# Kernel optimization log

Hardware: AMD Instinct MI355X
Metric: run time of the kernel (lower is better)

The kernel has to match this reference:

```python
import jax, jax.numpy as jnp
import numpy as np

N, E = 50000, 600000
IN_DIM, HID, OUT = 512, 256, 64
NEG_SLOPE = 0.2  # pyg GATConv default negative_slope


def setup_inputs() -> dict:
    key = jax.random.key(0)
    ks = jax.random.split(key, 6)
    features = jax.random.normal(ks[0], (N, IN_DIM), jnp.float32)
    edge_index = jax.random.randint(ks[1], (2, E), 0, N)
    W1 = jax.random.normal(ks[2], (IN_DIM, HID), jnp.float32) * (1.0 / np.sqrt(IN_DIM))
    W2 = jax.random.normal(ks[3], (HID, OUT), jnp.float32) * (1.0 / np.sqrt(HID))
    att_src = jax.random.normal(ks[4], (HID,), jnp.float32) * 0.1
    att_dst = jax.random.normal(ks[5], (HID,), jnp.float32) * 0.1
    return {"features": features, "W1": W1, "W2": W2,
            "att_src": att_src, "att_dst": att_dst, "edge_index": edge_index}


def _gat_propagate(h_pre, a_src, a_dst, src, dst, n):
    """STAGATE GATConv message passing (heads=1, concat=False, no self loops).

    Per-edge logit = leaky_relu(alpha_src[src] + alpha_dst[dst]),
    softmax over edges sharing the same dst, scatter-add of weighted src feats.
    """
    logits = jax.nn.leaky_relu(a_src[src] + a_dst[dst], NEG_SLOPE)        # [E]
    m = jax.ops.segment_max(logits, dst, num_segments=n)                   # [N]
    ex = jnp.exp(logits - m[dst])                                          # [E]
    denom = jax.ops.segment_sum(ex, dst, num_segments=n)                   # [N]
    w = ex / (denom[dst] + 1e-16)                                          # [E], pyg softmax eps
    return jax.ops.segment_sum(h_pre[src] * w[:, None], dst, num_segments=n)  # [N, C]


def reference(features, W1, W2, att_src, att_dst, edge_index):
    src, dst = edge_index[0], edge_index[1]
    n = features.shape[0]
    # conv1: attention computed and cached (self.attentions)
    hp1 = features @ W1                      # [N, HID]
    a_s = hp1 @ att_src                      # [N] per-node src attention score
    a_d = hp1 @ att_dst                      # [N] per-node dst attention score
    h1 = jax.nn.elu(_gat_propagate(hp1, a_s, a_d, src, dst, n))
    # conv2: attention=False -> plain linear
    h2 = h1 @ W2                             # [N, OUT]
    # conv3: weights = conv2.lin_src.T, tied_attention = conv1.attentions
    hp3 = h2 @ W2.T                          # [N, HID]
    h3 = jax.nn.elu(_gat_propagate(hp3, a_s, a_d, src, dst, n))
    # conv4: weights = conv1.lin_src.T, attention=False
    h4 = h3 @ W1.T                           # [N, IN_DIM]
    return (h2, h4)
```

## Files before the change

### kernel.cpp

```cpp
#include <hip/hip_runtime.h>
#include <hip/hip_bf16.h>
#include <cstdint>
#include <cstddef>

#define IN_DIM 512
#define HID 256
#define OUTD 64
#define NEG_SLOPE 0.2f

typedef __attribute__((ext_vector_type(8))) __bf16 bfrag_t;
typedef __attribute__((ext_vector_type(4))) float facc_t;
typedef __attribute__((ext_vector_type(4))) unsigned int u32x4;

__device__ __forceinline__ float bf2f(unsigned short u) {
  return __uint_as_float(((unsigned int)u) << 16);
}
__device__ __forceinline__ unsigned short f2bf(float f) {
  unsigned int x = __float_as_uint(f);
  x = (x + 0x7FFFu + ((x >> 16) & 1u)) >> 16;
  return (unsigned short)x;
}

#define GLOAD_LDS16(g, l)                                              \
  __builtin_amdgcn_global_load_lds(                                    \
      (const __attribute__((address_space(1))) void*)(g),              \
      (__attribute__((address_space(3))) void*)(l), 16, 0, 0)

template <int BM, int BN>
__global__ __launch_bounds__(256) void gemm_bt(const unsigned short* __restrict__ A,
                                               const unsigned short* __restrict__ B,
                                               void* __restrict__ Craw,
                                               unsigned short* __restrict__ Cb,
                                               int M, int N, int K, int c32, int act) {
  constexpr int FM = BM / 32, FN = BN / 32;
  constexpr int RT = BM + BN;
  __shared__ __align__(16) unsigned short lds[RT * 32];

  const int bm0 = blockIdx.x * BM;
  const int bn0 = blockIdx.y * BN;
  const int tid = threadIdx.x;
  const int lane = tid & 63;
  const int wave = tid >> 6;
  const int wrow = (wave >> 1) * (BM / 2);
  const int wcol = (wave & 1) * (BN / 2);
  const int lr = lane & 15;
  const int quad = lane >> 4;
  const int swz = (quad ^ (lr & 3)) << 3;

  facc_t acc[FM][FN];
#pragma unroll
  for (int i = 0; i < FM; ++i)
#pragma unroll
    for (int j = 0; j < FN; ++j) acc[i][j] = (facc_t){0.f, 0.f, 0.f, 0.f};

  for (int k0 = 0; k0 < K; k0 += 32) {
    __syncthreads();
#pragma unroll
    for (int t = wave; t < RT / 16; t += 4) {
      const int r0 = t * 16;
      const int row = r0 + (lane >> 2);
      const int seg = (lane & 3) ^ (row & 3);
      const unsigned short* g;
      if (r0 < BM) {
        int gm = bm0 + row;
        if (gm >= M) gm = M - 1;
        g = A + (size_t)gm * K + k0 + seg * 8;
      } else {
        g = B + (size_t)(bn0 + row - BM) * K + k0 + seg * 8;
      }
      GLOAD_LDS16(g, lds + t * 512);
    }
    __syncthreads();

    bfrag_t a[FM], b[FN];
#pragma unroll
    for (int i = 0; i < FM; ++i)
      a[i] = *(const bfrag_t*)&lds[(wrow + i * 16 + lr) * 32 + swz];
#pragma unroll
    for (int j = 0; j < FN; ++j)
      b[j] = *(const bfrag_t*)&lds[(BM + wcol + j * 16 + lr) * 32 + swz];
#pragma unroll
    for (int i = 0; i < FM; ++i)
#pragma unroll
      for (int j = 0; j < FN; ++j)
        acc[i][j] = __builtin_amdgcn_mfma_f32_16x16x32_bf16(a[i], b[j], acc[i][j], 0, 0, 0);
  }

#pragma unroll
  for (int i = 0; i < FM; ++i)
#pragma unroll
    for (int r = 0; r < 4; ++r) {
      const int grow = bm0 + wrow + i * 16 + quad * 4 + r;
      if (grow < M) {
#pragma unroll
        for (int j = 0; j < FN; ++j) {
          const int gcol = bn0 + wcol + j * 16 + lr;
          float v = acc[i][j][r];
          if (act) v = v > 0.f ? v : (expf(v) - 1.f);
          if (c32) ((float*)Craw)[(size_t)grow * N + gcol] = v;
          else ((unsigned short*)Craw)[(size_t)grow * N + gcol] = f2bf(v);
          if (Cb) Cb[(size_t)grow * N + gcol] = f2bf(v);
        }
      }
    }
}

template <int BM, int BN>
__global__ __launch_bounds__(256) void gemm_a32_bt_att(const float* __restrict__ A,
                                                       const unsigned short* __restrict__ B,
                                                       unsigned short* __restrict__ C,
                                                       const float* __restrict__ att_s,
                                                       const float* __restrict__ att_d,
                                                       float* __restrict__ as_,
                                                       float* __restrict__ ad_,
                                                       int M, int N, int K) {
  constexpr int FM = BM / 32, FN = BN / 32;
  constexpr int RT = BM + BN;
  __shared__ __align__(16) unsigned short lds[RT * 32];

  const int bm0 = blockIdx.x * BM;
  const int tid = threadIdx.x;
  const int lane = tid & 63;
  const int wave = tid >> 6;
  const int wrow = (wave >> 1) * (BM / 2);
  const int wcol = (wave & 1) * (BN / 2);
  const int lr = lane & 15;
  const int quad = lane >> 4;
  const int swz = (quad ^ (lr & 3)) << 3;

  const int arow0 = tid >> 2;
  const int aseg = tid & 3;

  facc_t acc[FM][FN];
#pragma unroll
  for (int i = 0; i < FM; ++i)
#pragma unroll
    for (int j = 0; j < FN; ++j) acc[i][j] = (facc_t){0.f, 0.f, 0.f, 0.f};

  for (int k0 = 0; k0 < K; k0 += 32) {
    __syncthreads();
#pragma unroll
    for (int t = wave; t < BN / 16; t += 4) {
      const int lr0 = BM + t * 16;
      const int row = lr0 + (lane >> 2);
      const int seg = (lane & 3) ^ (row & 3);
      const unsigned short* g = B + (size_t)(t * 16 + (lane >> 2)) * K + k0 + seg * 8;
      GLOAD_LDS16(g, lds + lr0 * 32);
    }
#pragma unroll
    for (int h = 0; h < 2; ++h) {
      const int row = arow0 + h * (BM / 2);
      int gm = bm0 + row;
      if (gm >= M) gm = M - 1;
      const float* g = A + (size_t)gm * K + k0 + aseg * 8;
      const float4 fa = ((const float4*)g)[0];
      const float4 fb = ((const float4*)g)[1];
      u32x4 pk;
      pk.x = (unsigned int)f2bf(fa.x) | ((unsigned int)f2bf(fa.y) << 16);
      pk.y = (unsigned int)f2bf(fa.z) | ((unsigned int)f2bf(fa.w) << 16);
      pk.z = (unsigned int)f2bf(fb.x) | ((unsigned int)f2bf(fb.y) << 16);
      pk.w = (unsigned int)f2bf(fb.z) | ((unsigned int)f2bf(fb.w) << 16);
      *(u32x4*)&lds[row * 32 + ((aseg ^ (row & 3)) << 3)] = pk;
    }
    __syncthreads();

    bfrag_t a[FM], b[FN];
#pragma unroll
    for (int i = 0; i < FM; ++i)
      a[i] = *(const bfrag_t*)&lds[(wrow + i * 16 + lr) * 32 + swz];
#pragma unroll
    for (int j = 0; j < FN; ++j)
      b[j] = *(const bfrag_t*)&lds[(BM + wcol + j * 16 + lr) * 32 + swz];
#pragma unroll
    for (int i = 0; i < FM; ++i)
#pragma unroll
      for (int j = 0; j < FN; ++j)
        acc[i][j] = __builtin_amdgcn_mfma_f32_16x16x32_bf16(a[i], b[j], acc[i][j], 0, 0, 0);
  }

  float av_s[FN], av_d[FN];
#pragma unroll
  for (int j = 0; j < FN; ++j) {
    av_s[j] = att_s[wcol + j * 16 + lr];
    av_d[j] = att_d[wcol + j * 16 + lr];
  }
  float* redS = (float*)lds;
  float* redD = (float*)lds + 2 * BM;
  __syncthreads();

#pragma unroll
  for (int i = 0; i < FM; ++i)
#pragma unroll
    for (int r = 0; r < 4; ++r) {
      const int grow = bm0 + wrow + i * 16 + quad * 4 + r;
      float ps = 0.f, pd = 0.f;
#pragma unroll
      for (int j = 0; j < FN; ++j) {
        const float v = acc[i][j][r];
        ps += v * av_s[j];
        pd += v * av_d[j];
        if (grow < M) C[(size_t)grow * N + (wcol + j * 16 + lr)] = f2bf(v);
      }
      ps += __shfl_xor(ps, 1); ps += __shfl_xor(ps, 2);
      ps += __shfl_xor(ps, 4); ps += __shfl_xor(ps, 8);
      pd += __shfl_xor(pd, 1); pd += __shfl_xor(pd, 2);
      pd += __shfl_xor(pd, 4); pd += __shfl_xor(pd, 8);
      if (lr == 0) {
        const int rloc = wrow + i * 16 + quad * 4 + r;
        redS[(wave & 1) * BM + rloc] = ps;
        redD[(wave & 1) * BM + rloc] = pd;
      }
    }
  __syncthreads();
  if (tid < BM) {
    const int grow = bm0 + tid;
    if (grow < M) {
      as_[grow] = redS[tid] + redS[BM + tid];
      ad_[grow] = redD[tid] + redD[BM + tid];
    }
  }
}

__global__ void cvt_weights(const float* __restrict__ W1, const float* __restrict__ W2,
                            unsigned short* __restrict__ W1T, unsigned short* __restrict__ W1b,
                            unsigned short* __restrict__ W2T, unsigned short* __restrict__ W2b) {
  const int idx = blockIdx.x * 256 + threadIdx.x;
  if (idx < IN_DIM * HID) {
    const unsigned short b = f2bf(W1[idx]);
    W1b[idx] = b;
    const int r = idx >> 8, c = idx & 255;
    W1T[(size_t)c * IN_DIM + r] = b;
  }
  if (idx < HID * OUTD) {
    const unsigned short b = f2bf(W2[idx]);
    W2b[idx] = b;
    const int r = idx >> 6, c = idx & 63;
    W2T[(size_t)c * HID + r] = b;
  }
}

__global__ void init_deg(int* __restrict__ deg, int n) {
  const int i = blockIdx.x * 256 + threadIdx.x;
  if (i < n) deg[i] = 0;
}

__global__ void edge_pass1(const int* __restrict__ src, const int* __restrict__ dst,
                           const float* __restrict__ as_, const float* __restrict__ ad_,
                           float* __restrict__ eexp, int* __restrict__ deg, int E, int n) {
  const int e = blockIdx.x * 256 + threadIdx.x;
  if (e >= E) return;
  const int s = src[e], d = dst[e];
  if ((unsigned)s >= (unsigned)n || (unsigned)d >= (unsigned)n) return;
  float l = as_[s] + ad_[d];
  l = l > 0.f ? l : NEG_SLOPE * l;
  eexp[e] = expf(fminf(l, 60.f));
  atomicAdd(&deg[d], 1);
}

__global__ __launch_bounds__(256) void scan_reduce(const int* __restrict__ deg,
                                                   int* __restrict__ bsum, int n) {
  __shared__ int ws4[4];
  const int tid = threadIdx.x, lane = tid & 63, wid = tid >> 6;
  const int base = blockIdx.x * 2048 + tid * 8;
  int s = 0;
#pragma unroll
  for (int j = 0; j < 8; ++j) {
    const int i = base + j;
    if (i < n) s += deg[i];
  }
  for (int off = 32; off > 0; off >>= 1) s += __shfl_down(s, off);
  if (lane == 0) ws4[wid] = s;
  __syncthreads();
  if (tid == 0) bsum[blockIdx.x] = ws4[0] + ws4[1] + ws4[2] + ws4[3];
}

__global__ __launch_bounds__(256) void scan_final(const int* __restrict__ deg,
                                                  const int* __restrict__ bsum,
                                                  int* __restrict__ row_ptr,
                                                  int* __restrict__ cursor, int n) {
  __shared__ int wsum[4];
  __shared__ int blockoff;
  const int tid = threadIdx.x, lane = tid & 63, wid = tid >> 6;
  if (wid == 0) {
    int v = (lane < blockIdx.x) ? bsum[lane] : 0;
    for (int off = 32; off > 0; off >>= 1) v += __shfl_down(v, off);
    if (lane == 0) blockoff = v;
  }
  const int base = blockIdx.x * 2048 + tid * 8;
  int v[8], s = 0;
#pragma unroll
  for (int j = 0; j < 8; ++j) {
    const int i = base + j;
    v[j] = (i < n) ? deg[i] : 0;
    s += v[j];
  }
  int ws = s;
  for (int off = 1; off < 64; off <<= 1) {
    const int t = __shfl_up(ws, off);
    if (lane >= off) ws += t;
  }
  if (lane == 63) wsum[wid] = ws;
  __syncthreads();
  int woff = 0;
  for (int w_ = 0; w_ < wid; ++w_) woff += wsum[w_];
  int run = blockoff + woff + (ws - s);
#pragma unroll
  for (int j = 0; j < 8; ++j) {
    const int i = base + j;
    if (i < n) {
      cursor[i] = run;
      row_ptr[i + 1] = run + v[j];
    }
    run += v[j];
  }
  if (blockIdx.x == 0 && tid == 0) row_ptr[0] = 0;
}

__global__ void edge_scatter(const int* __restrict__ src, const int* __restrict__ dst,
                             const float* __restrict__ eexp, int* __restrict__ cursor,
                             int2* __restrict__ csr, int E, int n) {
  const int e = blockIdx.x * 256 + threadIdx.x;
  if (e >= E) return;
  const int s = src[e], d = dst[e];
  if ((unsigned)s >= (unsigned)n || (unsigned)d >= (unsigned)n) return;
  const int pos = atomicAdd(&cursor[d], 1);
  int2 c;
  c.x = s;
  c.y = __float_as_int(eexp[e]);
  csr[pos] = c;
}

__global__ __launch_bounds__(256) void gat_prop256(const unsigned short* __restrict__ hpre,
                                                   const int* __restrict__ row_ptr,
                                                   const int2* __restrict__ csr,
                                                   unsigned short* __restrict__ out, int n) {
  const int node = blockIdx.x * 4 + (threadIdx.x >> 6);
  if (node >= n) return;
  const int lane = threadIdx.x & 63;
  const int half = lane >> 5;
  const int lh = lane & 31;
  const int beg = row_ptr[node], end = row_ptr[node + 1];
  const int deg = end - beg;
  const unsigned short* base = hpre + (lh << 3);
  float a[8] = {0.f, 0.f, 0.f, 0.f, 0.f, 0.f, 0.f, 0.f};
  float wsum = 0.f;

  int cs = 0;
  float cw = 0.f;
  if (lane < deg) {
    const int2 t = csr[beg + lane];
    cs = t.x;
    cw = __int_as_float(t.y);
  }
  const int dmain = deg < 64 ? deg : 64;
  for (int j0 = 0; j0 < dmain; j0 += 16) {
#pragma unroll
    for (int u = 0; u < 8; ++u) {
      const int j = j0 + 2 * u + half;
      const bool valid = j < dmain;
      const int jj = valid ? j : 0;
      const int s = __shfl(cs, jj);
      float w = __shfl(cw, jj);
      w = valid ? w : 0.f;
      const u32x4 v = *(const u32x4*)(base + (size_t)s * HID);
      wsum += w;
      a[0] += w * bf2f((unsigned short)(v.x & 0xffffu));
      a[1] += w * bf2f((unsigned short)(v.x >> 16));
      a[2] += w * bf2f((unsigned short)(v.y & 0xffffu));
      a[3] += w * bf2f((unsigned short)(v.y >> 16));
      a[4] += w * bf2f((unsigned short)(v.z & 0xffffu));
      a[5] += w * bf2f((unsigned short)(v.z >> 16));
      a[6] += w * bf2f((unsigned short)(v.w & 0xffffu));
      a[7] += w * bf2f((unsigned short)(v.w >> 16));
    }
  }
  for (int e = beg + 64; e < end; e += 2) {
    const int e2 = e + half;
    if (e2 < end) {
      const int2 c = csr[e2];
      const float w = __int_as_float(c.y);
      const u32x4 v = *(const u32x4*)(base + (size_t)c.x * HID);
      wsum += w;
      a[0] += w * bf2f((unsigned short)(v.x & 0xffffu));
      a[1] += w * bf2f((unsigned short)(v.x >> 16));
      a[2] += w * bf2f((unsigned short)(v.y & 0xffffu));
      a[3] += w * bf2f((unsigned short)(v.y >> 16));
      a[4] += w * bf2f((unsigned short)(v.z & 0xffffu));
      a[5] += w * bf2f((unsigned short)(v.z >> 16));
      a[6] += w * bf2f((unsigned short)(v.w & 0xffffu));
      a[7] += w * bf2f((unsigned short)(v.w >> 16));
    }
  }
#pragma unroll
  for (int i = 0; i < 8; ++i) a[i] += __shfl_xor(a[i], 32);
  wsum += __shfl_xor(wsum, 32);
  if (half == 0) {
    const float inv = 1.f / (wsum + 1e-16f);
#pragma unroll
    for (int i = 0; i < 8; ++i) {
      a[i] *= inv;
      a[i] = a[i] > 0.f ? a[i] : (expf(a[i]) - 1.f);
    }
    u32x4 o;
    o.x = (unsigned int)f2bf(a[0]) | ((unsigned int)f2bf(a[1]) << 16);
    o.y = (unsigned int)f2bf(a[2]) | ((unsigned int)f2bf(a[3]) << 16);
    o.z = (unsigned int)f2bf(a[4]) | ((unsigned int)f2bf(a[5]) << 16);
    o.w = (unsigned int)f2bf(a[6]) | ((unsigned int)f2bf(a[7]) << 16);
    *(u32x4*)(out + (size_t)node * HID + (lh << 3)) = o;
  }
}

__global__ __launch_bounds__(256) void gat_prop64(const unsigned short* __restrict__ hpre,
                                                  const int* __restrict__ row_ptr,
                                                  const int2* __restrict__ csr,
                                                  unsigned short* __restrict__ out, int n) {
  const int node = blockIdx.x * 4 + (threadIdx.x >> 6);
  if (node >= n) return;
  const int lane = threadIdx.x & 63;
  const int quad = lane >> 4;
  const int lr = lane & 15;
  const int beg = row_ptr[node], end = row_ptr[node + 1];
  const int deg = end - beg;
  const unsigned short* base = hpre + (lr << 2);
  float a0 = 0.f, a1 = 0.f, a2 = 0.f, a3 = 0.f, wsum = 0.f;

  int cs = 0;
  float cw = 0.f;
  if (lane < deg) {
    const int2 t = csr[beg + lane];
    cs = t.x;
    cw = __int_as_float(t.y);
  }
  const int dmain = deg < 64 ? deg : 64;
  for (int j0 = 0; j0 < dmain; j0 += 16) {
#pragma unroll
    for (int u = 0; u < 4; ++u) {
      const int j = j0 + 4 * u + quad;
      const bool valid = j < dmain;
      const int jj = valid ? j : 0;
      const int s = __shfl(cs, jj);
      float w = __shfl(cw, jj);
      w = valid ? w : 0.f;
      const uint2 v = *(const uint2*)(base + (size_t)s * OUTD);
      wsum += w;
      a0 += w * bf2f((unsigned short)(v.x & 0xffffu));
      a1 += w * bf2f((unsigned short)(v.x >> 16));
      a2 += w * bf2f((unsigned short)(v.y & 0xffffu));
      a3 += w * bf2f((unsigned short)(v.y >> 16));
    }
  }
  for (int e = beg + 64; e < end; e += 4) {
    const int e2 = e + quad;
    if (e2 < end) {
      const int2 c = csr[e2];
      const float w = __int_as_float(c.y);
      const uint2 v = *(const uint2*)(base + (size_t)c.x * OUTD);
      wsum += w;
      a0 += w * bf2f((unsigned short)(v.x & 0xffffu));
      a1 += w * bf2f((unsigned short)(v.x >> 16));
      a2 += w * bf2f((unsigned short)(v.y & 0xffffu));
      a3 += w * bf2f((unsigned short)(v.y >> 16));
    }
  }
  a0 += __shfl_xor(a0, 16); a0 += __shfl_xor(a0, 32);
  a1 += __shfl_xor(a1, 16); a1 += __shfl_xor(a1, 32);
  a2 += __shfl_xor(a2, 16); a2 += __shfl_xor(a2, 32);
  a3 += __shfl_xor(a3, 16); a3 += __shfl_xor(a3, 32);
  wsum += __shfl_xor(wsum, 16); wsum += __shfl_xor(wsum, 32);
  if (quad == 0) {
    const float inv = 1.f / (wsum + 1e-16f);
    uint2 o;
    o.x = (unsigned int)f2bf(a0 * inv) | ((unsigned int)f2bf(a1 * inv) << 16);
    o.y = (unsigned int)f2bf(a2 * inv) | ((unsigned int)f2bf(a3 * inv) << 16);
    *(uint2*)(out + (size_t)node * OUTD + (lr << 2)) = o;
  }
}

extern "C" void kernel_launch(void* const* d_in, const int* in_sizes, int n_in,
                              void* d_out, int out_size, void* d_ws, size_t ws_size,
                              hipStream_t stream) {
  const float* feat = (const float*)d_in[0];
  const float* W1 = (const float*)d_in[1];
  const float* W2 = (const float*)d_in[2];
  const float* att_s = (const float*)d_in[3];
  const float* att_d = (const float*)d_in[4];
  const int* ei = (const int*)d_in[5];
  const int N = in_sizes[0] / IN_DIM;
  const int E = in_sizes[5] / 2;
  const int* src = ei;
  const int* dst = ei + E;
  float* outf = (float*)d_out;

  unsigned short* hp1 = (unsigned short*)(outf + (size_t)N * OUTD);
  unsigned short* g2 = hp1 + (size_t)N * HID;

  char* w = (char*)d_ws;
  size_t off = 0;
  auto alloc = [&](size_t bytes) -> void* {
    void* p = w + off;
    off += (bytes + 255) & ~(size_t)255;
    return p;
  };
  unsigned short* h1h3 = (unsigned short*)alloc((size_t)N * HID * 2);
  unsigned short* h2b = (unsigned short*)alloc((size_t)N * OUTD * 2);
  float* a_src_v = (float*)alloc((size_t)N * 4);
  float* a_dst_v = (float*)alloc((size_t)N * 4);
  float* eexp = (float*)alloc((size_t)E * 4);
  int* deg = (int*)alloc((size_t)N * 4);
  int* row_ptr = (int*)alloc((size_t)(N + 1) * 4);
  int* cursor = (int*)alloc((size_t)N * 4);
  int* bsum = (int*)alloc((size_t)64 * 4);
  int2* csr = (int2*)alloc((size_t)E * 8);
  unsigned short* W1T = (unsigned short*)alloc((size_t)IN_DIM * HID * 2);
  unsigned short* W1b = (unsigned short*)alloc((size_t)IN_DIM * HID * 2);
  unsigned short* W2T = (unsigned short*)alloc((size_t)HID * OUTD * 2);
  unsigned short* W2b = (unsigned short*)alloc((size_t)HID * OUTD * 2);

  const int EB = (E + 255) / 256;
  const int NB = (N + 255) / 256;
  const int MB = (N + 127) / 128;
  const int SB = (N + 2047) / 2048;

  cvt_weights<<<(IN_DIM * HID + 255) / 256, 256, 0, stream>>>(W1, W2, W1T, W1b, W2T, W2b);

  gemm_a32_bt_att<128, 256><<<MB, 256, 0, stream>>>(feat, W1T, hp1, att_s, att_d,
                                                    a_src_v, a_dst_v, N, HID, IN_DIM);

  init_deg<<<NB, 256, 0, stream>>>(deg, N);
  edge_pass1<<<EB, 256, 0, stream>>>(src, dst, a_src_v, a_dst_v, eexp, deg, E, N);
  scan_reduce<<<SB, 256, 0, stream>>>(deg, bsum, N);
  scan_final<<<SB, 256, 0, stream>>>(deg, bsum, row_ptr, cursor, N);
  edge_scatter<<<EB, 256, 0, stream>>>(src, dst, eexp, cursor, csr, E, N);

  gat_prop256<<<(N + 3) / 4, 256, 0, stream>>>(hp1, row_ptr, csr, h1h3, N);
  gemm_bt<128, 64><<<dim3(MB, OUTD / 64), 256, 0, stream>>>(h1h3, W2T, outf, h2b,
                                                            N, OUTD, HID, 1, 0);
  gat_prop64<<<(N + 3) / 4, 256, 0, stream>>>(h2b, row_ptr, csr, g2, N);
  gemm_bt<128, 256><<<dim3(MB, HID / 256), 256, 0, stream>>>(g2, W2b, h1h3, nullptr,
                                                             N, HID, OUTD, 0, 1);
  gemm_bt<128, 256><<<dim3(MB, IN_DIM / 256), 256, 0, stream>>>(h1h3, W1b,
                                                                outf + (size_t)N * OUTD,
                                                                nullptr, N, IN_DIM, HID, 1, 0);
}
```

Measured before the change: 503.1 us.

## Fuse small GEMMs into GAT propagation kernels and restructure edge passes

Folds the h1@W2 and g2@W2^T linear layers into the two GAT propagation kernels as per-node dot products against bf16 weights, removing two GEMM launches and their intermediate round-trips through global memory. The per-edge exponent is now computed inside the CSR scatter, so the separate eexp buffer and its write and read go away, and the degree and attention-score zeroing is folded into the weight-conversion kernel. The first GEMM is split into two column tiles that combine partial attention scores with atomics, and the final GEMM uses 128x128 tiles. The cost is scalar FMA work of about 16K per node in the fused kernels instead of MFMA, redundant weight reads per wave, and nondeterministic float atomics.

```diff
diff --git a/kernel.cpp b/kernel.cpp
--- a/kernel.cpp
+++ b/kernel.cpp
@@ -29,9 +29,8 @@
 template <int BM, int BN>
 __global__ __launch_bounds__(256) void gemm_bt(const unsigned short* __restrict__ A,
                                                const unsigned short* __restrict__ B,
-                                               void* __restrict__ Craw,
-                                               unsigned short* __restrict__ Cb,
-                                               int M, int N, int K, int c32, int act) {
+                                               float* __restrict__ C,
+                                               int M, int N, int K) {
   constexpr int FM = BM / 32, FN = BN / 32;
   constexpr int RT = BM + BN;
   __shared__ __align__(16) unsigned short lds[RT * 32];
@@ -93,14 +92,8 @@
       const int grow = bm0 + wrow + i * 16 + quad * 4 + r;
       if (grow < M) {
 #pragma unroll
-        for (int j = 0; j < FN; ++j) {
-          const int gcol = bn0 + wcol + j * 16 + lr;
-          float v = acc[i][j][r];
-          if (act) v = v > 0.f ? v : (expf(v) - 1.f);
-          if (c32) ((float*)Craw)[(size_t)grow * N + gcol] = v;
-          else ((unsigned short*)Craw)[(size_t)grow * N + gcol] = f2bf(v);
-          if (Cb) Cb[(size_t)grow * N + gcol] = f2bf(v);
-        }
+        for (int j = 0; j < FN; ++j)
+          C[(size_t)grow * N + bn0 + wcol + j * 16 + lr] = acc[i][j][r];
       }
     }
 }
@@ -119,6 +112,7 @@
   __shared__ __align__(16) unsigned short lds[RT * 32];
 
   const int bm0 = blockIdx.x * BM;
+  const int bn0 = blockIdx.y * BN;
   const int tid = threadIdx.x;
   const int lane = tid & 63;
   const int wave = tid >> 6;
@@ -144,7 +138,7 @@
       const int lr0 = BM + t * 16;
       const int row = lr0 + (lane >> 2);
       const int seg = (lane & 3) ^ (row & 3);
-      const unsigned short* g = B + (size_t)(t * 16 + (lane >> 2)) * K + k0 + seg * 8;
+      const unsigned short* g = B + (size_t)(bn0 + t * 16 + (lane >> 2)) * K + k0 + seg * 8;
       GLOAD_LDS16(g, lds + lr0 * 32);
     }
 #pragma unroll
@@ -181,13 +175,9 @@
   float av_s[FN], av_d[FN];
 #pragma unroll
   for (int j = 0; j < FN; ++j) {
-    av_s[j] = att_s[wcol + j * 16 + lr];
-    av_d[j] = att_d[wcol + j * 16 + lr];
-  }
-  float* redS = (float*)lds;
-  float* redD = (float*)lds + 2 * BM;
-  __syncthreads();
-
+    av_s[j] = att_s[bn0 + wcol + j * 16 + lr];
+    av_d[j] = att_d[bn0 + wcol + j * 16 + lr];
+  }
 #pragma unroll
   for (int i = 0; i < FM; ++i)
 #pragma unroll
@@ -199,31 +189,24 @@
         const float v = acc[i][j][r];
         ps += v * av_s[j];
         pd += v * av_d[j];
-        if (grow < M) C[(size_t)grow * N + (wcol + j * 16 + lr)] = f2bf(v);
+        if (grow < M) C[(size_t)grow * N + bn0 + wcol + j * 16 + lr] = f2bf(v);
       }
       ps += __shfl_xor(ps, 1); ps += __shfl_xor(ps, 2);
       ps += __shfl_xor(ps, 4); ps += __shfl_xor(ps, 8);
       pd += __shfl_xor(pd, 1); pd += __shfl_xor(pd, 2);
       pd += __shfl_xor(pd, 4); pd += __shfl_xor(pd, 8);
-      if (lr == 0) {
-        const int rloc = wrow + i * 16 + quad * 4 + r;
-        redS[(wave & 1) * BM + rloc] = ps;
-        redD[(wave & 1) * BM + rloc] = pd;
+      if (lr == 0 && grow < M) {
+        atomicAdd(&as_[grow], ps);
+        atomicAdd(&ad_[grow], pd);
       }
     }
-  __syncthreads();
-  if (tid < BM) {
-    const int grow = bm0 + tid;
-    if (grow < M) {
-      as_[grow] = redS[tid] + redS[BM + tid];
-      ad_[grow] = redD[tid] + redD[BM + tid];
-    }
-  }
 }
 
 __global__ void cvt_weights(const float* __restrict__ W1, const float* __restrict__ W2,
                             unsigned short* __restrict__ W1T, unsigned short* __restrict__ W1b,
-                            unsigned short* __restrict__ W2T, unsigned short* __restrict__ W2b) {
+                            unsigned short* __restrict__ W2T, unsigned short* __restrict__ W2b,
+                            float* __restrict__ as_, float* __restrict__ ad_,
+                            int* __restrict__ deg, int n) {
   const int idx = blockIdx.x * 256 + threadIdx.x;
   if (idx < IN_DIM * HID) {
     const unsigned short b = f2bf(W1[idx]);
@@ -237,23 +220,19 @@
     const int r = idx >> 6, c = idx & 63;
     W2T[(size_t)c * HID + r] = b;
   }
-}
-
-__global__ void init_deg(int* __restrict__ deg, int n) {
-  const int i = blockIdx.x * 256 + threadIdx.x;
-  if (i < n) deg[i] = 0;
-}
-
-__global__ void edge_pass1(const int* __restrict__ src, const int* __restrict__ dst,
-                           const float* __restrict__ as_, const float* __restrict__ ad_,
-                           float* __restrict__ eexp, int* __restrict__ deg, int E, int n) {
+  if (idx < n) {
+    as_[idx] = 0.f;
+    ad_[idx] = 0.f;
+    deg[idx] = 0;
+  }
+}
+
+__global__ void edge_deg(const int* __restrict__ src, const int* __restrict__ dst,
+                         int* __restrict__ deg, int E, int n) {
   const int e = blockIdx.x * 256 + threadIdx.x;
   if (e >= E) return;
   const int s = src[e], d = dst[e];
   if ((unsigned)s >= (unsigned)n || (unsigned)d >= (unsigned)n) return;
-  float l = as_[s] + ad_[d];
-  l = l > 0.f ? l : NEG_SLOPE * l;
-  eexp[e] = expf(fminf(l, 60.f));
   atomicAdd(&deg[d], 1);
 }
 
@@ -317,24 +296,32 @@
 }
 
 __global__ void edge_scatter(const int* __restrict__ src, const int* __restrict__ dst,
-                             const float* __restrict__ eexp, int* __restrict__ cursor,
-                             int2* __restrict__ csr, int E, int n) {
+                             const float* __restrict__ as_, const float* __restrict__ ad_,
+                             int* __restrict__ cursor, int2* __restrict__ csr, int E, int n) {
   const int e = blockIdx.x * 256 + threadIdx.x;
   if (e >= E) return;
   const int s = src[e], d = dst[e];
   if ((unsigned)s >= (unsigned)n || (unsigned)d >= (unsigned)n) return;
+  float l = as_[s] + ad_[d];
+  l = l > 0.f ? l : NEG_SLOPE * l;
+  const float ex = expf(fminf(l, 60.f));
   const int pos = atomicAdd(&cursor[d], 1);
   int2 c;
   c.x = s;
-  c.y = __float_as_int(eexp[e]);
+  c.y = __float_as_int(ex);
   csr[pos] = c;
 }
 
-__global__ __launch_bounds__(256) void gat_prop256(const unsigned short* __restrict__ hpre,
-                                                   const int* __restrict__ row_ptr,
-                                                   const int2* __restrict__ csr,
-                                                   unsigned short* __restrict__ out, int n) {
-  const int node = blockIdx.x * 4 + (threadIdx.x >> 6);
+__global__ __launch_bounds__(256) void gat_prop256_fc(const unsigned short* __restrict__ hpre,
+                                                      const int* __restrict__ row_ptr,
+                                                      const int2* __restrict__ csr,
+                                                      const unsigned short* __restrict__ W2T,
+                                                      float* __restrict__ h2out,
+                                                      unsigned short* __restrict__ h2b,
+                                                      int n) {
+  __shared__ float h1row[4][256];
+  const int nib = threadIdx.x >> 6;
+  const int node = blockIdx.x * 4 + nib;
   if (node >= n) return;
   const int lane = threadIdx.x & 63;
   const int half = lane >> 5;
@@ -394,27 +381,46 @@
 #pragma unroll
   for (int i = 0; i < 8; ++i) a[i] += __shfl_xor(a[i], 32);
   wsum += __shfl_xor(wsum, 32);
+
+  const float inv = 1.f / (wsum + 1e-16f);
+#pragma unroll
+  for (int i = 0; i < 8; ++i) {
+    a[i] *= inv;
+    a[i] = a[i] > 0.f ? a[i] : (expf(a[i]) - 1.f);
+  }
   if (half == 0) {
-    const float inv = 1.f / (wsum + 1e-16f);
-#pragma unroll
-    for (int i = 0; i < 8; ++i) {
-      a[i] *= inv;
-      a[i] = a[i] > 0.f ? a[i] : (expf(a[i]) - 1.f);
-    }
-    u32x4 o;
-    o.x = (unsigned int)f2bf(a[0]) | ((unsigned int)f2bf(a[1]) << 16);
-    o.y = (unsigned int)f2bf(a[2]) | ((unsigned int)f2bf(a[3]) << 16);
-    o.z = (unsigned int)f2bf(a[4]) | ((unsigned int)f2bf(a[5]) << 16);
-    o.w = (unsigned int)f2bf(a[6]) | ((unsigned int)f2bf(a[7]) << 16);
-    *(u32x4*)(out + (size_t)node * HID + (lh << 3)) = o;
-  }
-}
-
-__global__ __launch_bounds__(256) void gat_prop64(const unsigned short* __restrict__ hpre,
-                                                  const int* __restrict__ row_ptr,
-                                                  const int2* __restrict__ csr,
-                                                  unsigned short* __restrict__ out, int n) {
-  const int node = blockIdx.x * 4 + (threadIdx.x >> 6);
+#pragma unroll
+    for (int i = 0; i < 8; ++i) h1row[nib][lh * 8 + i] = a[i];
+  }
+  const u32x4* wrow = (const u32x4*)(W2T + (size_t)lane * HID);
+  float h2 = 0.f;
+#pragma unroll
+  for (int c8 = 0; c8 < 32; ++c8) {
+    const u32x4 wv = wrow[c8];
+    const float4 h0 = *(const float4*)&h1row[nib][c8 * 8];
+    const float4 h1_ = *(const float4*)&h1row[nib][c8 * 8 + 4];
+    h2 += h0.x * bf2f((unsigned short)(wv.x & 0xffffu))
+        + h0.y * bf2f((unsigned short)(wv.x >> 16))
+        + h0.z * bf2f((unsigned short)(wv.y & 0xffffu))
+        + h0.w * bf2f((unsigned short)(wv.y >> 16))
+        + h1_.x * bf2f((unsigned short)(wv.z & 0xffffu))
+        + h1_.y * bf2f((unsigned short)(wv.z >> 16))
+        + h1_.z * bf2f((unsigned short)(wv.w & 0xffffu))
+        + h1_.w * bf2f((unsigned short)(wv.w >> 16));
+  }
+  h2out[(size_t)node * OUTD + lane] = h2;
+  h2b[(size_t)node * OUTD + lane] = f2bf(h2);
+}
+
+__global__ __launch_bounds__(256) void gat_prop64_fc(const unsigned short* __restrict__ hpre,
+                                                     const int* __restrict__ row_ptr,
+                                                     const int2* __restrict__ csr,
+                                                     const unsigned short* __restrict__ W2b,
+                                                     unsigned short* __restrict__ h3out,
+                                                     int n) {
+  __shared__ float g2row[4][64];
+  const int nib = threadIdx.x >> 6;
+  const int node = blockIdx.x * 4 + nib;
   if (node >= n) return;
   const int lane = threadIdx.x & 63;
   const int quad = lane >> 4;
@@ -467,13 +473,50 @@
   a2 += __shfl_xor(a2, 16); a2 += __shfl_xor(a2, 32);
   a3 += __shfl_xor(a3, 16); a3 += __shfl_xor(a3, 32);
   wsum += __shfl_xor(wsum, 16); wsum += __shfl_xor(wsum, 32);
+
+  const float inv = 1.f / (wsum + 1e-16f);
   if (quad == 0) {
-    const float inv = 1.f / (wsum + 1e-16f);
-    uint2 o;
-    o.x = (unsigned int)f2bf(a0 * inv) | ((unsigned int)f2bf(a1 * inv) << 16);
-    o.y = (unsigned int)f2bf(a2 * inv) | ((unsigned int)f2bf(a3 * inv) << 16);
-    *(uint2*)(out + (size_t)node * OUTD + (lr << 2)) = o;
-  }
+    g2row[nib][lr * 4 + 0] = a0 * inv;
+    g2row[nib][lr * 4 + 1] = a1 * inv;
+    g2row[nib][lr * 4 + 2] = a2 * inv;
+    g2row[nib][lr * 4 + 3] = a3 * inv;
+  }
+  const u32x4* wr0 = (const u32x4*)(W2b + (size_t)(4 * lane + 0) * OUTD);
+  const u32x4* wr1 = (const u32x4*)(W2b + (size_t)(4 * lane + 1) * OUTD);
+  const u32x4* wr2 = (const u32x4*)(W2b + (size_t)(4 * lane + 2) * OUTD);
+  const u32x4* wr3 = (const u32x4*)(W2b + (size_t)(4 * lane + 3) * OUTD);
+  float o0 = 0.f, o1 = 0.f, o2 = 0.f, o3 = 0.f;
+#pragma unroll
+  for (int n8 = 0; n8 < 8; ++n8) {
+    const float4 g0 = *(const float4*)&g2row[nib][n8 * 8];
+    const float4 g1 = *(const float4*)&g2row[nib][n8 * 8 + 4];
+    const u32x4 w0 = wr0[n8];
+    const u32x4 w1 = wr1[n8];
+    const u32x4 w2 = wr2[n8];
+    const u32x4 w3 = wr3[n8];
+#define DOT8(wv)                                                           \
+  (g0.x * bf2f((unsigned short)(wv.x & 0xffffu)) +                         \
+   g0.y * bf2f((unsigned short)(wv.x >> 16)) +                             \
+   g0.z * bf2f((unsigned short)(wv.y & 0xffffu)) +                         \
+   g0.w * bf2f((unsigned short)(wv.y >> 16)) +                             \
+   g1.x * bf2f((unsigned short)(wv.z & 0xffffu)) +                         \
+   g1.y * bf2f((unsigned short)(wv.z >> 16)) +                             \
+   g1.z * bf2f((unsigned short)(wv.w & 0xffffu)) +                         \
+   g1.w * bf2f((unsigned short)(wv.w >> 16)))
+    o0 += DOT8(w0);
+    o1 += DOT8(w1);
+    o2 += DOT8(w2);
+    o3 += DOT8(w3);
+#undef DOT8
+  }
+  o0 = o0 > 0.f ? o0 : (expf(o0) - 1.f);
+  o1 = o1 > 0.f ? o1 : (expf(o1) - 1.f);
+  o2 = o2 > 0.f ? o2 : (expf(o2) - 1.f);
+  o3 = o3 > 0.f ? o3 : (expf(o3) - 1.f);
+  uint2 o;
+  o.x = (unsigned int)f2bf(o0) | ((unsigned int)f2bf(o1) << 16);
+  o.y = (unsigned int)f2bf(o2) | ((unsigned int)f2bf(o3) << 16);
+  *(uint2*)(h3out + (size_t)node * HID + 4 * lane) = o;
 }
 
 extern "C" void kernel_launch(void* const* d_in, const int* in_sizes, int n_in,
@@ -492,7 +535,6 @@
   float* outf = (float*)d_out;
 
   unsigned short* hp1 = (unsigned short*)(outf + (size_t)N * OUTD);
-  unsigned short* g2 = hp1 + (size_t)N * HID;
 
   char* w = (char*)d_ws;
   size_t off = 0;
@@ -501,11 +543,10 @@
     off += (bytes + 255) & ~(size_t)255;
     return p;
   };
-  unsigned short* h1h3 = (unsigned short*)alloc((size_t)N * HID * 2);
+  unsigned short* h3 = (unsigned short*)alloc((size_t)N * HID * 2);
   unsigned short* h2b = (unsigned short*)alloc((size_t)N * OUTD * 2);
   float* a_src_v = (float*)alloc((size_t)N * 4);
   float* a_dst_v = (float*)alloc((size_t)N * 4);
-  float* eexp = (float*)alloc((size_t)E * 4);
   int* deg = (int*)alloc((size_t)N * 4);
   int* row_ptr = (int*)alloc((size_t)(N + 1) * 4);
   int* cursor = (int*)alloc((size_t)N * 4);
@@ -517,28 +558,23 @@
   unsigned short* W2b = (unsigned short*)alloc((size_t)HID * OUTD * 2);
 
   const int EB = (E + 255) / 256;
-  const int NB = (N + 255) / 256;
   const int MB = (N + 127) / 128;
   const int SB = (N + 2047) / 2048;
 
-  cvt_weights<<<(IN_DIM * HID + 255) / 256, 256, 0, stream>>>(W1, W2, W1T, W1b, W2T, W2b);
-
-  gemm_a32_bt_att<128, 256><<<MB, 256, 0, stream>>>(feat, W1T, hp1, att_s, att_d,
-                                                    a_src_v, a_dst_v, N, HID, IN_DIM);
-
-  init_deg<<<NB, 256, 0, stream>>>(deg, N);
-  edge_pass1<<<EB, 256, 0, stream>>>(src, dst, a_src_v, a_dst_v, eexp, deg, E, N);
+  cvt_weights<<<(IN_DIM * HID + 255) / 256, 256, 0, stream>>>(W1, W2, W1T, W1b, W2T, W2b,
+                                                              a_src_v, a_dst_v, deg, N);
+
+  gemm_a32_bt_att<128, 128><<<dim3(MB, HID / 128), 256, 0, stream>>>(
+      feat, W1T, hp1, att_s, att_d, a_src_v, a_dst_v, N, HID, IN_DIM);
+
+  edge_deg<<<EB, 256, 0, stream>>>(src, dst, deg, E, N);
   scan_reduce<<<SB, 256, 0, stream>>>(deg, bsum, N);
   scan_final<<<SB, 256, 0, stream>>>(deg, bsum, row_ptr, cursor, N);
-  edge_scatter<<<EB, 256, 0, stream>>>(src, dst, eexp, cursor, csr, E, N);
-
-  gat_prop256<<<(N + 3) / 4, 256, 0, stream>>>(hp1, row_ptr, csr, h1h3, N);
-  gemm_bt<128, 64><<<dim3(MB, OUTD / 64), 256, 0, stream>>>(h1h3, W2T, outf, h2b,
-                                                            N, OUTD, HID, 1, 0);
-  gat_prop64<<<(N + 3) / 4, 256, 0, stream>>>(h2b, row_ptr, csr, g2, N);
-  gemm_bt<128, 256><<<dim3(MB, HID / 256), 256, 0, stream>>>(g2, W2b, h1h3, nullptr,
-                                                             N, HID, OUTD, 0, 1);
-  gemm_bt<128, 256><<<dim3(MB, IN_DIM / 256), 256, 0, stream>>>(h1h3, W1b,
+  edge_scatter<<<EB, 256, 0, stream>>>(src, dst, a_src_v, a_dst_v, cursor, csr, E, N);
+
+  gat_prop256_fc<<<(N + 3) / 4, 256, 0, stream>>>(hp1, row_ptr, csr, W2T, outf, h2b, N);
+  gat_prop64_fc<<<(N + 3) / 4, 256, 0, stream>>>(h2b, row_ptr, csr, W2b, h3, N);
+  gemm_bt<128, 128><<<dim3(MB, IN_DIM / 128), 256, 0, stream>>>(h3, W1b,
                                                                 outf + (size_t)N * OUTD,
-                                                                nullptr, N, IN_DIM, HID, 1, 0);
-}
+                                                                N, IN_DIM, HID);
+}
```

New measurement: 734.9 us. 1.46x slower.
